# Optimization experiments

Measured on AMD Instinct MI355X. Metric: run time of the kernel, lower is better.

The kernel has to match this reference:

```python
import jax, jax.numpy as jnp
import numpy as np

B, K, N = 131072, 512, 1024  # batch, message bits, code bits


def setup_inputs() -> dict:
    key = jax.random.key(0)
    k1, k2 = jax.random.split(key)
    input_data = jax.random.randint(k1, (B, K), 0, 2).astype(jnp.float32)
    generator_matrix = jax.random.randint(k2, (N, K), 0, 2).astype(jnp.float32)
    return {"input_data": input_data, "generator_matrix": generator_matrix}


def reference(input_data, generator_matrix):
    # GF(2) encoding: (x @ G^T) mod 2
    # input_data: [B, K], generator_matrix: [N, K] -> out [B, N]
    prod = jnp.matmul(input_data, generator_matrix.T)
    return jnp.mod(prod, 2.0)
```

## Files before the change

kernel.cpp:

```cpp
#include <hip/hip_runtime.h>
#include <cstdint>


typedef float f32x4 __attribute__((ext_vector_type(4)));

__global__ void pack256_kernel(const float* __restrict__ in,
                               unsigned long long* __restrict__ out,
                               int nChunks) {
    const int chunk = blockIdx.x * (blockDim.x >> 6) + (threadIdx.x >> 6);
    const int lane = threadIdx.x & 63;
    if (chunk >= nChunks) return;
    const float4 v =
        reinterpret_cast<const float4*>(in + (size_t)chunk * 256)[lane];
    unsigned long long m0 = __ballot(v.x != 0.0f);
    unsigned long long m1 = __ballot(v.y != 0.0f);
    unsigned long long m2 = __ballot(v.z != 0.0f);
    unsigned long long m3 = __ballot(v.w != 0.0f);
    if (lane == 0) {
        unsigned long long* o = out + (size_t)chunk * 4;
        o[0] = m0; o[1] = m1; o[2] = m2; o[3] = m3;
    }
}

__global__ __launch_bounds__(256, 5) void gf2_fused_kernel(
    const float* __restrict__ x,
    const uint32_t* __restrict__ gp,
    float* __restrict__ out) {
    __shared__ uint32_t xl[64 * 16];

    const int tid = threadIdx.x;
    const int lane = tid & 63;
    const int wv = tid >> 6;
    const long long b0 = (long long)blockIdx.x * 64;

    uint32_t g[4][16];
#pragma unroll
    for (int j = 0; j < 4; ++j) {
        const uint4* gr =
            reinterpret_cast<const uint4*>(gp + (size_t)(tid * 4 + j) * 16);
        uint4 a = gr[0], b = gr[1], c = gr[2], d = gr[3];
        g[j][0] = a.x;  g[j][1] = a.y;  g[j][2] = a.z;  g[j][3] = a.w;
        g[j][4] = b.x;  g[j][5] = b.y;  g[j][6] = b.z;  g[j][7] = b.w;
        g[j][8] = c.x;  g[j][9] = c.y;  g[j][10] = c.z; g[j][11] = c.w;
        g[j][12] = d.x; g[j][13] = d.y; g[j][14] = d.z; g[j][15] = d.w;
    }

    {
        const float* xr = x + (b0 + wv * 16) * 512 + lane * 4;
        float4 p0 = *reinterpret_cast<const float4*>(xr);
        float4 p1 = *reinterpret_cast<const float4*>(xr + 256);
        for (int r = 0; r < 16; ++r) {
            const float4 c0 = p0, c1 = p1;
            if (r < 15) {
                xr += 512;
                p0 = *reinterpret_cast<const float4*>(xr);
                p1 = *reinterpret_cast<const float4*>(xr + 256);
            }
            unsigned long long m0 = __ballot(c0.x != 0.0f);
            unsigned long long m1 = __ballot(c0.y != 0.0f);
            unsigned long long m2 = __ballot(c0.z != 0.0f);
            unsigned long long m3 = __ballot(c0.w != 0.0f);
            unsigned long long m4 = __ballot(c1.x != 0.0f);
            unsigned long long m5 = __ballot(c1.y != 0.0f);
            unsigned long long m6 = __ballot(c1.z != 0.0f);
            unsigned long long m7 = __ballot(c1.w != 0.0f);
            if (lane == 0) {
                uint4* dst = reinterpret_cast<uint4*>(&xl[(wv * 16 + r) * 16]);
                dst[0] = make_uint4((uint32_t)m0, (uint32_t)(m0 >> 32),
                                    (uint32_t)m1, (uint32_t)(m1 >> 32));
                dst[1] = make_uint4((uint32_t)m2, (uint32_t)(m2 >> 32),
                                    (uint32_t)m3, (uint32_t)(m3 >> 32));
                dst[2] = make_uint4((uint32_t)m4, (uint32_t)(m4 >> 32),
                                    (uint32_t)m5, (uint32_t)(m5 >> 32));
                dst[3] = make_uint4((uint32_t)m6, (uint32_t)(m6 >> 32),
                                    (uint32_t)m7, (uint32_t)(m7 >> 32));
            }
        }
    }
    __syncthreads();

    for (int r = 0; r < 64; ++r) {
        const uint4* xr4 = reinterpret_cast<const uint4*>(&xl[r * 16]);
        uint4 q0 = xr4[0], q1 = xr4[1], q2 = xr4[2], q3 = xr4[3];
        const uint32_t xv[16] = {q0.x, q0.y, q0.z, q0.w,
                                 q1.x, q1.y, q1.z, q1.w,
                                 q2.x, q2.y, q2.z, q2.w,
                                 q3.x, q3.y, q3.z, q3.w};
        uint32_t a0 = 0, a1 = 0, a2 = 0, a3 = 0;
#pragma unroll
        for (int i = 0; i < 16; ++i) {
            a0 ^= xv[i] & g[0][i];
            a1 ^= xv[i] & g[1][i];
            a2 ^= xv[i] & g[2][i];
            a3 ^= xv[i] & g[3][i];
        }
        f32x4 o;
        o.x = (float)(__popc(a0) & 1);
        o.y = (float)(__popc(a1) & 1);
        o.z = (float)(__popc(a2) & 1);
        o.w = (float)(__popc(a3) & 1);
        __builtin_nontemporal_store(
            o, reinterpret_cast<f32x4*>(out + (size_t)(b0 + r) * 1024) + tid);
    }
}

extern "C" void kernel_launch(void* const* d_in, const int* in_sizes, int n_in,
                              void* d_out, int out_size, void* d_ws, size_t ws_size,
                              hipStream_t stream) {
    const float* x = (const float*)d_in[0];
    const float* G = (const float*)d_in[1];
    float* out = (float*)d_out;

    const int B = 131072;
    unsigned long long* gp64 = (unsigned long long*)d_ws;

    pack256_kernel<<<512, 256, 0, stream>>>(G, gp64, 2048);
    gf2_fused_kernel<<<B / 64, 256, 0, stream>>>(
        x, (const uint32_t*)gp64, out);
}
```

Before: 156.8 us.

## Double-buffer packed x rows and overlap second tile's loads with first tile's compute

Each block now handles 128 batch rows in two 64-row halves using two LDS buffers. While the first half is computed and stored, the global loads and ballot-packing for the second half are interleaved every fourth row. This hides the x-load latency behind compute and halves the number of blocks, so the per-block G register load happens half as often. It adds register pressure from the prefetch registers and gives fewer blocks for load balancing.

```diff
diff --git a/kernel.cpp b/kernel.cpp
--- a/kernel.cpp
+++ b/kernel.cpp
@@ -26,12 +26,12 @@
     const float* __restrict__ x,
     const uint32_t* __restrict__ gp,
     float* __restrict__ out) {
-    __shared__ uint32_t xl[64 * 16];
+    __shared__ uint32_t xl[2][64 * 16];
 
     const int tid = threadIdx.x;
     const int lane = tid & 63;
     const int wv = tid >> 6;
-    const long long b0 = (long long)blockIdx.x * 64;
+    const long long b0 = (long long)blockIdx.x * 128;
 
     uint32_t g[4][16];
 #pragma unroll
@@ -45,6 +45,76 @@
         g[j][12] = d.x; g[j][13] = d.y; g[j][14] = d.z; g[j][15] = d.w;
     }
 
+#define PACKROW(buf, dstrow, c0, c1)                                        \
+    do {                                                                    \
+        unsigned long long m0 = __ballot(c0.x != 0.0f);                     \
+        unsigned long long m1 = __ballot(c0.y != 0.0f);                     \
+        unsigned long long m2 = __ballot(c0.z != 0.0f);                     \
+        unsigned long long m3 = __ballot(c0.w != 0.0f);                     \
+        unsigned long long m4 = __ballot(c1.x != 0.0f);                     \
+        unsigned long long m5 = __ballot(c1.y != 0.0f);                     \
+        unsigned long long m6 = __ballot(c1.z != 0.0f);                     \
+        unsigned long long m7 = __ballot(c1.w != 0.0f);                     \
+        if (lane == 0) {                                                    \
+            uint4* dst = reinterpret_cast<uint4*>(&xl[buf][(dstrow)*16]);   \
+            dst[0] = make_uint4((uint32_t)m0, (uint32_t)(m0 >> 32),         \
+                                (uint32_t)m1, (uint32_t)(m1 >> 32));        \
+            dst[1] = make_uint4((uint32_t)m2, (uint32_t)(m2 >> 32),         \
+                                (uint32_t)m3, (uint32_t)(m3 >> 32));        \
+            dst[2] = make_uint4((uint32_t)m4, (uint32_t)(m4 >> 32),         \
+                                (uint32_t)m5, (uint32_t)(m5 >> 32));        \
+            dst[3] = make_uint4((uint32_t)m6, (uint32_t)(m6 >> 32),         \
+                                (uint32_t)m7, (uint32_t)(m7 >> 32));        \
+        }                                                                   \
+    } while (0)
+
+#define COMPUTE(buf, rr, gr_row)                                            \
+    do {                                                                    \
+        const uint4* xr4 = reinterpret_cast<const uint4*>(&xl[buf][(rr)*16]); \
+        uint4 q0 = xr4[0], q1 = xr4[1];                                     \
+        uint32_t a0, a1, a2, a3;                                            \
+        a0 = q0.x & g[0][0];  a1 = q0.x & g[1][0];                          \
+        a2 = q0.x & g[2][0];  a3 = q0.x & g[3][0];                          \
+        a0 ^= q0.y & g[0][1]; a1 ^= q0.y & g[1][1];                         \
+        a2 ^= q0.y & g[2][1]; a3 ^= q0.y & g[3][1];                         \
+        a0 ^= q0.z & g[0][2]; a1 ^= q0.z & g[1][2];                         \
+        a2 ^= q0.z & g[2][2]; a3 ^= q0.z & g[3][2];                         \
+        a0 ^= q0.w & g[0][3]; a1 ^= q0.w & g[1][3];                         \
+        a2 ^= q0.w & g[2][3]; a3 ^= q0.w & g[3][3];                         \
+        a0 ^= q1.x & g[0][4]; a1 ^= q1.x & g[1][4];                         \
+        a2 ^= q1.x & g[2][4]; a3 ^= q1.x & g[3][4];                         \
+        a0 ^= q1.y & g[0][5]; a1 ^= q1.y & g[1][5];                         \
+        a2 ^= q1.y & g[2][5]; a3 ^= q1.y & g[3][5];                         \
+        a0 ^= q1.z & g[0][6]; a1 ^= q1.z & g[1][6];                         \
+        a2 ^= q1.z & g[2][6]; a3 ^= q1.z & g[3][6];                         \
+        a0 ^= q1.w & g[0][7]; a1 ^= q1.w & g[1][7];                         \
+        a2 ^= q1.w & g[2][7]; a3 ^= q1.w & g[3][7];                         \
+        q0 = xr4[2]; q1 = xr4[3];                                           \
+        a0 ^= q0.x & g[0][8];  a1 ^= q0.x & g[1][8];                        \
+        a2 ^= q0.x & g[2][8];  a3 ^= q0.x & g[3][8];                        \
+        a0 ^= q0.y & g[0][9];  a1 ^= q0.y & g[1][9];                        \
+        a2 ^= q0.y & g[2][9];  a3 ^= q0.y & g[3][9];                        \
+        a0 ^= q0.z & g[0][10]; a1 ^= q0.z & g[1][10];                       \
+        a2 ^= q0.z & g[2][10]; a3 ^= q0.z & g[3][10];                       \
+        a0 ^= q0.w & g[0][11]; a1 ^= q0.w & g[1][11];                       \
+        a2 ^= q0.w & g[2][11]; a3 ^= q0.w & g[3][11];                       \
+        a0 ^= q1.x & g[0][12]; a1 ^= q1.x & g[1][12];                       \
+        a2 ^= q1.x & g[2][12]; a3 ^= q1.x & g[3][12];                       \
+        a0 ^= q1.y & g[0][13]; a1 ^= q1.y & g[1][13];                       \
+        a2 ^= q1.y & g[2][13]; a3 ^= q1.y & g[3][13];                       \
+        a0 ^= q1.z & g[0][14]; a1 ^= q1.z & g[1][14];                       \
+        a2 ^= q1.z & g[2][14]; a3 ^= q1.z & g[3][14];                       \
+        a0 ^= q1.w & g[0][15]; a1 ^= q1.w & g[1][15];                       \
+        a2 ^= q1.w & g[2][15]; a3 ^= q1.w & g[3][15];                       \
+        f32x4 o;                                                            \
+        o.x = (float)(__popc(a0) & 1);                                      \
+        o.y = (float)(__popc(a1) & 1);                                      \
+        o.z = (float)(__popc(a2) & 1);                                      \
+        o.w = (float)(__popc(a3) & 1);                                      \
+        __builtin_nontemporal_store(                                        \
+            o, reinterpret_cast<f32x4*>(out + (size_t)(gr_row)*1024) + tid);\
+    } while (0)
+
     {
         const float* xr = x + (b0 + wv * 16) * 512 + lane * 4;
         float4 p0 = *reinterpret_cast<const float4*>(xr);
@@ -56,52 +126,39 @@
                 p0 = *reinterpret_cast<const float4*>(xr);
                 p1 = *reinterpret_cast<const float4*>(xr + 256);
             }
-            unsigned long long m0 = __ballot(c0.x != 0.0f);
-            unsigned long long m1 = __ballot(c0.y != 0.0f);
-            unsigned long long m2 = __ballot(c0.z != 0.0f);
-            unsigned long long m3 = __ballot(c0.w != 0.0f);
-            unsigned long long m4 = __ballot(c1.x != 0.0f);
-            unsigned long long m5 = __ballot(c1.y != 0.0f);
-            unsigned long long m6 = __ballot(c1.z != 0.0f);
-            unsigned long long m7 = __ballot(c1.w != 0.0f);
-            if (lane == 0) {
-                uint4* dst = reinterpret_cast<uint4*>(&xl[(wv * 16 + r) * 16]);
-                dst[0] = make_uint4((uint32_t)m0, (uint32_t)(m0 >> 32),
-                                    (uint32_t)m1, (uint32_t)(m1 >> 32));
-                dst[1] = make_uint4((uint32_t)m2, (uint32_t)(m2 >> 32),
-                                    (uint32_t)m3, (uint32_t)(m3 >> 32));
-                dst[2] = make_uint4((uint32_t)m4, (uint32_t)(m4 >> 32),
-                                    (uint32_t)m5, (uint32_t)(m5 >> 32));
-                dst[3] = make_uint4((uint32_t)m6, (uint32_t)(m6 >> 32),
-                                    (uint32_t)m7, (uint32_t)(m7 >> 32));
+            PACKROW(0, wv * 16 + r, c0, c1);
+        }
+    }
+    const float* xr1 = x + (b0 + 64 + wv * 16) * 512 + lane * 4;
+    float4 pf0 = *reinterpret_cast<const float4*>(xr1);
+    float4 pf1 = *reinterpret_cast<const float4*>(xr1 + 256);
+    __syncthreads();
+
+    {
+        int k = 0;
+#pragma unroll 4
+        for (int r = 0; r < 64; ++r) {
+            COMPUTE(0, r, b0 + r);
+            if ((r & 3) == 3) {
+                const float4 c0 = pf0, c1 = pf1;
+                if (k < 15) {
+                    xr1 += 512;
+                    pf0 = *reinterpret_cast<const float4*>(xr1);
+                    pf1 = *reinterpret_cast<const float4*>(xr1 + 256);
+                }
+                PACKROW(1, wv * 16 + k, c0, c1);
+                ++k;
             }
         }
     }
     __syncthreads();
 
+#pragma unroll 2
     for (int r = 0; r < 64; ++r) {
-        const uint4* xr4 = reinterpret_cast<const uint4*>(&xl[r * 16]);
-        uint4 q0 = xr4[0], q1 = xr4[1], q2 = xr4[2], q3 = xr4[3];
-        const uint32_t xv[16] = {q0.x, q0.y, q0.z, q0.w,
-                                 q1.x, q1.y, q1.z, q1.w,
-                                 q2.x, q2.y, q2.z, q2.w,
-                                 q3.x, q3.y, q3.z, q3.w};
-        uint32_t a0 = 0, a1 = 0, a2 = 0, a3 = 0;
-#pragma unroll
-        for (int i = 0; i < 16; ++i) {
-            a0 ^= xv[i] & g[0][i];
-            a1 ^= xv[i] & g[1][i];
-            a2 ^= xv[i] & g[2][i];
-            a3 ^= xv[i] & g[3][i];
-        }
-        f32x4 o;
-        o.x = (float)(__popc(a0) & 1);
-        o.y = (float)(__popc(a1) & 1);
-        o.z = (float)(__popc(a2) & 1);
-        o.w = (float)(__popc(a3) & 1);
-        __builtin_nontemporal_store(
-            o, reinterpret_cast<f32x4*>(out + (size_t)(b0 + r) * 1024) + tid);
+        COMPUTE(1, r, b0 + 64 + r);
     }
+#undef PACKROW
+#undef COMPUTE
 }
 
 extern "C" void kernel_launch(void* const* d_in, const int* in_sizes, int n_in,
@@ -115,6 +172,6 @@
     unsigned long long* gp64 = (unsigned long long*)d_ws;
 
     pack256_kernel<<<512, 256, 0, stream>>>(G, gp64, 2048);
-    gf2_fused_kernel<<<B / 64, 256, 0, stream>>>(
+    gf2_fused_kernel<<<B / 128, 256, 0, stream>>>(
         x, (const uint32_t*)gp64, out);
 }
```

New measurement: 316.9 us. +102.1%, slower.
